# Kernel optimization log

Hardware: AMD Instinct MI355X
Metric: run time of the kernel (lower is better)

The kernel has to match this reference:

```python
import jax, jax.numpy as jnp
import numpy as np

V, D, L, H, S, B = 32000, 512, 4, 8, 2048, 2
HD = D // H
FF = 4 * D
EPS = 1e-5


def _ln(x, w, b):
    m = jnp.mean(x, axis=-1, keepdims=True)
    v = jnp.var(x, axis=-1, keepdims=True)
    return (x - m) / jnp.sqrt(v + EPS) * w + b


def setup_inputs() -> dict:
    key = jax.random.key(0)
    ks = jax.random.split(key, 32)
    rn = lambda k, shape, s=0.02: jax.random.normal(k, shape, jnp.float32) * s
    return {
        'x': jax.random.randint(ks[0], (B, S), 0, V),
        'tok_emb': rn(ks[1], (V, D)),
        'pos_emb': rn(ks[2], (S, D)),
        'qw': rn(ks[3], (L, D, D)), 'qb': rn(ks[4], (L, D)),
        'kw': rn(ks[5], (L, D, D)), 'kb': rn(ks[6], (L, D)),
        'vw': rn(ks[7], (L, D, D)), 'vb': rn(ks[8], (L, D)),
        'ow': rn(ks[9], (L, D, D)), 'ob': rn(ks[10], (L, D)),
        'qphase': rn(ks[11], (L, H), 0.1),
        'sp_phase': rn(ks[12], (L, D), 0.1),
        'n1w': jnp.ones((L, D), jnp.float32), 'n1b': jnp.zeros((L, D), jnp.float32),
        'n2w': jnp.ones((L, D), jnp.float32), 'n2b': jnp.zeros((L, D), jnp.float32),
        'f1w': rn(ks[13], (L, D, FF)), 'f1b': rn(ks[14], (L, FF)),
        'f2w': rn(ks[15], (L, FF, D)), 'f2b': rn(ks[16], (L, D)),
        'iw': rn(ks[17], (L, D, D)), 'ib': rn(ks[18], (L, D)),
        'gw': rn(ks[19], (L, D, D)), 'gb': rn(ks[20], (L, D)),
        'nw': jnp.ones((D,), jnp.float32), 'nb': jnp.zeros((D,), jnp.float32),
        'outw': rn(ks[21], (D, V)), 'outb': rn(ks[22], (V,)),
    }


def _forward(x, tok_emb, pos_emb, qw, qb, kw, kb, vw, vb, ow, ob, qphase, sp_phase,
             n1w, n1b, n2w, n2b, f1w, f1b, f2w, f2b, iw, ib, gw, gb, nw, nb, outw, outb):
    Bx, Sx = x.shape
    h = tok_emb[x] + pos_emb[:Sx][None, :, :]          # [B,S,D]
    mask = jnp.tril(jnp.ones((Sx, Sx), dtype=bool))    # causal
    scale = 1.0 / np.sqrt(HD).astype(np.float32)
    for l in range(L):
        # quantum attention with phase-modulated scores
        hn = _ln(h, n1w[l], n1b[l])
        q = (hn @ qw[l] + qb[l]).reshape(Bx, Sx, H, HD)
        k = (hn @ kw[l] + kb[l]).reshape(Bx, Sx, H, HD)
        v = (hn @ vw[l] + vb[l]).reshape(Bx, Sx, H, HD)
        scores = jnp.einsum('bqhd,bkhd->bhqk', q, k) * scale
        qi = jnp.cos(qphase[l][None, :, None, None] * scores)
        scores = scores * (1.0 + 0.1 * qi)
        scores = jnp.where(mask[None, None], scores, -jnp.inf)
        attn = jax.nn.softmax(scores, axis=-1)
        o = jnp.einsum('bhqk,bkhd->bqhd', attn, v).reshape(Bx, Sx, D)
        h = h + o @ ow[l] + ob[l]
        # superposition: x * cos(phase * x)
        h = h * jnp.cos(sp_phase[l] * h)
        # feed-forward (exact GELU, as torch default)
        hn2 = _ln(h, n2w[l], n2b[l])
        h = h + jax.nn.gelu(hn2 @ f1w[l] + f1b[l], approximate=False) @ f2w[l] + f2b[l]
        # interference gate
        g = jax.nn.sigmoid(h @ gw[l] + gb[l])
        h = (h @ iw[l] + ib[l]) * g + h * (1.0 - g)
    h = _ln(h, nw, nb)
    return h @ outw + outb                              # [B,S,V] logits


def reference(x, tok_emb, pos_emb, qw, qb, kw, kb, vw, vb, ow, ob, qphase, sp_phase,
              n1w, n1b, n2w, n2b, f1w, f1b, f2w, f2b, iw, ib, gw, gb, nw, nb, outw, outb):
    return _forward(x, tok_emb, pos_emb, qw, qb, kw, kb, vw, vb, ow, ob, qphase, sp_phase,
                    n1w, n1b, n2w, n2b, f1w, f1b, f2w, f2b, iw, ib, gw, gb, nw, nb, outw, outb)
```

## Files before the change

### kernel.cpp

```cpp
#include <hip/hip_runtime.h>
#include <math.h>

#define DIM 512
#define NH 8
#define HD 64
#define SEQ 2048
#define BATCH 2
#define NLAYER 4
#define FFD 2048
#define VOCAB 32000
#define ROWS (BATCH*SEQ)
#define QKV_LD 1536

typedef unsigned short u16;
typedef __attribute__((ext_vector_type(8))) short bfrag;
typedef __attribute__((ext_vector_type(4))) short sfrag4;
typedef __attribute__((ext_vector_type(4))) float facc;

__device__ __forceinline__ u16 f2bf(float f){
  unsigned u = __builtin_bit_cast(unsigned, f);
  u += 0x7fff + ((u>>16)&1);
  return (u16)(u>>16);
}

typedef __attribute__((address_space(3))) unsigned int lds_u32;
typedef const __attribute__((address_space(1))) unsigned int glob_u32;
__device__ __forceinline__ void gload16(const void* g, void* l){
  __builtin_amdgcn_global_load_lds((glob_u32*)g, (lds_u32*)l, 16, 0, 0);
}

template<int N> __device__ __forceinline__ void wait_vmcnt(){
  if constexpr (N==0)       asm volatile("s_waitcnt vmcnt(0)" ::: "memory");
  else if constexpr (N==3)  asm volatile("s_waitcnt vmcnt(3)" ::: "memory");
  else if constexpr (N==4)  asm volatile("s_waitcnt vmcnt(4)" ::: "memory");
  else if constexpr (N==6)  asm volatile("s_waitcnt vmcnt(6)" ::: "memory");
  else if constexpr (N==8)  asm volatile("s_waitcnt vmcnt(8)" ::: "memory");
  else if constexpr (N==16) asm volatile("s_waitcnt vmcnt(16)" ::: "memory");
  else static_assert(N==0, "unsupported vmcnt");
}

__device__ __forceinline__ void do_transpose(
    const float* __restrict__ I, u16* __restrict__ O,
    int K, int N, int nx, int ky, int imode){
  __shared__ float t[32][33];
  const int n0 = nx*32, k0 = ky*32;
  #pragma unroll
  for (int i=0;i<4;i++){
    int k = k0 + threadIdx.y + 8*i;
    t[threadIdx.y+8*i][threadIdx.x] = I[(size_t)k*N + n0 + threadIdx.x];
  }
  __syncthreads();
  #pragma unroll
  for (int i=0;i<4;i++){
    int n = n0 + threadIdx.y + 8*i;
    int np = (imode==0) ? n : ((n>>4)*32 + (n&15) + (imode==2 ? 16 : 0));
    O[(size_t)np*K + k0 + threadIdx.x] = f2bf(t[threadIdx.x][threadIdx.y+8*i]);
  }
}

__global__ void pre_all(
    const float* qw, const float* kw, const float* vw, const float* ow,
    const float* iw, const float* gw, const float* f1w, const float* f2w,
    const float* outw,
    const float* qb, const float* kb, const float* vb,
    const float* ib, const float* gb,
    u16* qkvT, u16* owT, u16* igT, u16* f1T, u16* f2T, u16* outT,
    float* qkvb, float* igb){
  const int bid = blockIdx.x;
  if (bid < 6144){
    int job = bid >> 10, local = bid & 1023;
    int l = local >> 8, rr = local & 255;
    int nx = rr & 15, ky = rr >> 4;
    const float* src; u16* dst; int im = 0;
    switch(job){
      case 0: src=qw+(size_t)l*262144; dst=qkvT+(size_t)l*786432;        break;
      case 1: src=kw+(size_t)l*262144; dst=qkvT+(size_t)l*786432+262144; break;
      case 2: src=vw+(size_t)l*262144; dst=qkvT+(size_t)l*786432+524288; break;
      case 3: src=ow+(size_t)l*262144; dst=owT +(size_t)l*262144;        break;
      case 4: src=iw+(size_t)l*262144; dst=igT +(size_t)l*524288; im=1;  break;
      default:src=gw+(size_t)l*262144; dst=igT +(size_t)l*524288; im=2;  break;
    }
    do_transpose(src, dst, 512, 512, nx, ky, im);
  } else if (bid < 10240){
    int local = bid - 6144;
    int l = local >> 10, rr = local & 1023;
    int nx = rr & 63, ky = rr >> 6;
    do_transpose(f1w+(size_t)l*1048576, f1T+(size_t)l*1048576, 512, 2048, nx, ky, 0);
  } else if (bid < 14336){
    int local = bid - 10240;
    int l = local >> 10, rr = local & 1023;
    int nx = rr & 15, ky = rr >> 4;
    do_transpose(f2w+(size_t)l*1048576, f2T+(size_t)l*1048576, 2048, 512, nx, ky, 0);
  } else if (bid < 30336){
    int local = bid - 14336;
    int nx = local % 1000, ky = local / 1000;
    do_transpose(outw, outT, 512, 32000, nx, ky, 0);
  } else if (bid < 30360){
    int tid = threadIdx.y*32 + threadIdx.x;
    int idx = (bid-30336)*256 + tid;
    int l = idx/1536, r2 = idx%1536;
    qkvb[idx] = (r2<512) ? qb[l*512+r2] : (r2<1024 ? kb[l*512+r2-512] : vb[l*512+r2-1024]);
  } else {
    int tid = threadIdx.y*32 + threadIdx.x;
    int idx = (bid-30360)*256 + tid;
    int l = idx>>10, cp = idx&1023;
    int bb = cp>>4, c = (bb>>1)*16 + (cp&15);
    igb[idx] = (bb&1) ? gb[l*512+c] : ib[l*512+c];
  }
}

__global__ void embed_k(const int* __restrict__ x, const float* __restrict__ tok,
                        const float* __restrict__ pos, float* __restrict__ h){
  int idx = blockIdx.x*256 + threadIdx.x;
  int row = idx >> 7;
  int d4  = idx & 127;
  int s   = row & (SEQ-1);
  int tkn = x[row];
  float4 tv = *(const float4*)(tok + (size_t)tkn*DIM + d4*4);
  float4 pv = *(const float4*)(pos + (size_t)s*DIM + d4*4);
  float4 r; r.x=tv.x+pv.x; r.y=tv.y+pv.y; r.z=tv.z+pv.z; r.w=tv.w+pv.w;
  *(float4*)(h + (size_t)row*DIM + d4*4) = r;
}

__global__ __launch_bounds__(256) void ln_k(const float* __restrict__ h,
    const float* __restrict__ w, const float* __restrict__ bsc,
    u16* __restrict__ out){
  const int wid = threadIdx.x>>6, lane = threadIdx.x&63;
  const int row = blockIdx.x*4 + wid;
  const float* r = h + (size_t)row*DIM + lane*8;
  float4 v0 = *(const float4*)r;
  float4 v1 = *(const float4*)(r+4);
  float s  = v0.x+v0.y+v0.z+v0.w + v1.x+v1.y+v1.z+v1.w;
  float ss = v0.x*v0.x+v0.y*v0.y+v0.z*v0.z+v0.w*v0.w
           + v1.x*v1.x+v1.y*v1.y+v1.z*v1.z+v1.w*v1.w;
  #pragma unroll
  for (int m=1;m<64;m<<=1){ s += __shfl_xor(s,m); ss += __shfl_xor(ss,m); }
  const float mean = s*(1.f/DIM);
  const float var  = ss*(1.f/DIM) - mean*mean;
  const float rsd  = rsqrtf(var + 1e-5f);
  float4 w0 = *(const float4*)(w + lane*8);
  float4 w1 = *(const float4*)(w + lane*8 + 4);
  float4 b0 = *(const float4*)(bsc + lane*8);
  float4 b1 = *(const float4*)(bsc + lane*8 + 4);
  bfrag pk;
  pk[0]=(short)f2bf((v0.x-mean)*rsd*w0.x+b0.x);
  pk[1]=(short)f2bf((v0.y-mean)*rsd*w0.y+b0.y);
  pk[2]=(short)f2bf((v0.z-mean)*rsd*w0.z+b0.z);
  pk[3]=(short)f2bf((v0.w-mean)*rsd*w0.w+b0.w);
  pk[4]=(short)f2bf((v1.x-mean)*rsd*w1.x+b1.x);
  pk[5]=(short)f2bf((v1.y-mean)*rsd*w1.y+b1.y);
  pk[6]=(short)f2bf((v1.z-mean)*rsd*w1.z+b1.z);
  pk[7]=(short)f2bf((v1.w-mean)*rsd*w1.w+b1.w);
  *(bfrag*)&out[(size_t)row*DIM + lane*8] = pk;
}

template<int BM,int BN,int BK,int WRN,int WCN,int DEPTH,int MODE,int SWZ>
__global__ __launch_bounds__(WRN*WCN*64, 2) void gemm_p(
    const u16* __restrict__ A, const u16* __restrict__ BT,
    const float* __restrict__ bias, const float* __restrict__ aux,
    float* __restrict__ Cf, u16* __restrict__ Cb, u16* __restrict__ vt,
    int M, int N, int K){
  constexpr int NTH = WRN*WCN*64;
  constexpr int FI  = BM/(16*WRN);
  constexpr int FJ  = BN/(16*WCN);
  constexpr int CPR = BK/8;
  constexpr int LA  = BM*CPR/NTH;
  constexpr int LB  = BN*CPR/NTH;
  constexpr int LPT = LA+LB;
  constexpr int NKK = BK/32;
  extern __shared__ __align__(16) u16 smem[];
  u16* lds_a = smem;
  u16* lds_b = smem + DEPTH*BM*BK;

  const int tid = threadIdx.x;
  const int wid = tid>>6, lane = tid&63;
  const int wr = wid / WCN, wc = wid % WCN;
  const int lr = lane&15, lg = lane>>4;
  int tm, tn;
  if constexpr (SWZ){
    const unsigned nwg = gridDim.x*gridDim.y;
    const unsigned lin = blockIdx.y*gridDim.x + blockIdx.x;
    const unsigned q = nwg >> 3;
    const unsigned sw = (lin & 7)*q + (lin >> 3);
    tm = sw % gridDim.x; tn = sw / gridDim.x;
  } else {
    tm = blockIdx.x; tn = blockIdx.y;
  }

  auto swzf = [](int row)->int{ return (BK==64) ? (row&7) : ((row>>1)&3); };

  auto stage = [&](int t, int buf){
    const int k0 = t*BK;
    #pragma unroll
    for (int i=0;i<LA;i++){
      int u = i*NTH + tid;
      int row = u/CPR, c = (u%CPR) ^ swzf(row);
      gload16(&A[(size_t)(tm*BM+row)*K + k0 + c*8], &lds_a[buf*BM*BK + u*8]);
    }
    #pragma unroll
    for (int i=0;i<LB;i++){
      int u = i*NTH + tid;
      int row = u/CPR, c = (u%CPR) ^ swzf(row);
      gload16(&BT[(size_t)(tn*BN+row)*K + k0 + c*8], &lds_b[buf*BN*BK + u*8]);
    }
  };

  facc acc[FI][FJ] = {};
  const int NT = K/BK;
  stage(0,0);
  if (NT>1) stage(1,1);
  if constexpr (DEPTH==3) { if (NT>2) stage(2,2); }
  for (int t=0;t<NT;t++){
    const int buf = t % DEPTH;
    const u16* la = &lds_a[buf*BM*BK];
    const u16* lb = &lds_b[buf*BN*BK];
    const int rem = NT-1-t;
    if constexpr (DEPTH==3){
      if (rem >= 2) wait_vmcnt<2*LPT>();
      else if (rem == 1) wait_vmcnt<LPT>();
      else wait_vmcnt<0>();
    } else {
      if (rem >= 1) wait_vmcnt<LPT>(); else wait_vmcnt<0>();
    }
    __builtin_amdgcn_s_barrier();
    __builtin_amdgcn_sched_barrier(0);
    bfrag af[FI], bf[FJ];
    #pragma unroll
    for (int i=0;i<FI;i++){
      int row = wr*(FI*16) + i*16 + lr;
      af[i] = *(const bfrag*)&la[row*BK + ((lg ^ swzf(row))*8)];
    }
    #pragma unroll
    for (int j=0;j<FJ;j++){
      int row = wc*(FJ*16) + j*16 + lr;
      bf[j] = *(const bfrag*)&lb[row*BK + ((lg ^ swzf(row))*8)];
    }
    if constexpr (NKK==1){
      asm volatile("s_waitcnt lgkmcnt(0)" ::: "memory");
      __builtin_amdgcn_sched_barrier(0);
      __builtin_amdgcn_s_barrier();
      __builtin_amdgcn_sched_barrier(0);
      if (t+DEPTH<NT) stage(t+DEPTH, buf);
      __builtin_amdgcn_s_setprio(1);
      #pragma unroll
      for (int i=0;i<FI;i++)
        #pragma unroll
        for (int j=0;j<FJ;j++)
          acc[i][j] = __builtin_amdgcn_mfma_f32_16x16x32_bf16(af[i], bf[j], acc[i][j],0,0,0);
      __builtin_amdgcn_s_setprio(0);
    } else {
      __builtin_amdgcn_s_setprio(1);
      #pragma unroll
      for (int i=0;i<FI;i++)
        #pragma unroll
        for (int j=0;j<FJ;j++)
          acc[i][j] = __builtin_amdgcn_mfma_f32_16x16x32_bf16(af[i], bf[j], acc[i][j],0,0,0);
      __builtin_amdgcn_s_setprio(0);
      bfrag af1[FI], bf1[FJ];
      #pragma unroll
      for (int i=0;i<FI;i++){
        int row = wr*(FI*16) + i*16 + lr;
        af1[i] = *(const bfrag*)&la[row*BK + (((4+lg) ^ swzf(row))*8)];
      }
      #pragma unroll
      for (int j=0;j<FJ;j++){
        int row = wc*(FJ*16) + j*16 + lr;
        bf1[j] = *(const bfrag*)&lb[row*BK + (((4+lg) ^ swzf(row))*8)];
      }
      asm volatile("s_waitcnt lgkmcnt(0)" ::: "memory");
      __builtin_amdgcn_sched_barrier(0);
      __builtin_amdgcn_s_barrier();
      __builtin_amdgcn_sched_barrier(0);
      if (t+DEPTH<NT) stage(t+DEPTH, buf);
      __builtin_amdgcn_s_setprio(1);
      #pragma unroll
      for (int i=0;i<FI;i++)
        #pragma unroll
        for (int j=0;j<FJ;j++)
          acc[i][j] = __builtin_amdgcn_mfma_f32_16x16x32_bf16(af1[i], bf1[j], acc[i][j],0,0,0);
      __builtin_amdgcn_s_setprio(0);
    }
  }

  if constexpr (MODE==5){
    #pragma unroll
    for (int i=0;i<FI;i++){
      #pragma unroll
      for (int j=0;j<FJ;j+=2){
        const int colp = tn*BN + wc*(FJ*16) + j*16;
        const int c = (colp>>5)*16 + lr;
        const float bi = bias[colp + lr];
        const float bg = bias[colp + 16 + lr];
        #pragma unroll
        for (int r=0;r<4;r++){
          const int row = tm*BM + wr*(FI*16) + i*16 + lg*4 + r;
          float vi = acc[i][j][r]   + bi;
          float vg = acc[i][j+1][r] + bg;
          float g  = 1.f/(1.f+__expf(-vg));
          const size_t o = (size_t)row*DIM + c;
          float hv = Cf[o];
          Cf[o] = vi*g + hv*(1.f-g);
        }
      }
    }
  } else if constexpr (MODE==7){
    #pragma unroll
    for (int i=0;i<FI;i++){
      #pragma unroll
      for (int j=0;j<FJ;j++){
        const int colblk = tn*BN + wc*(FJ*16) + j*16;
        const float bv = bias[colblk + lr];
        if (colblk < 1024){
          #pragma unroll
          for (int r=0;r<4;r++){
            const int row = tm*BM + wr*(FI*16) + i*16 + lg*4 + r;
            Cb[(size_t)row*N + colblk + lr] = f2bf(acc[i][j][r] + bv);
          }
        } else {
          const int c = colblk + lr - 1024;
          const int hh = c>>6, d = c&63;
          const int row0 = tm*BM + wr*(FI*16) + i*16 + lg*4;
          const int b = row0>>11, s0 = row0&2047;
          sfrag4 pk;
          #pragma unroll
          for (int r=0;r<4;r++) pk[r] = (short)f2bf(acc[i][j][r] + bv);
          *(sfrag4*)&vt[((size_t)((b*NH+hh)*HD + d))*SEQ + s0] = pk;
        }
      }
    }
  } else {
    #pragma unroll
    for (int i=0;i<FI;i++){
      #pragma unroll
      for (int j=0;j<FJ;j++){
        const int col = tn*BN + wc*(FJ*16) + j*16 + lr;
        const float bv = bias ? bias[col] : 0.f;
        #pragma unroll
        for (int r=0;r<4;r++){
          const int row = tm*BM + wr*(FI*16) + i*16 + lg*4 + r;
          float v = acc[i][j][r] + bv;
          const size_t o = (size_t)row*N + col;
          if      (MODE==0) Cf[o] = v;
          else if (MODE==8) __builtin_nontemporal_store(v, &Cf[o]);
          else if (MODE==3){ float g = 0.5f*v*(1.f+erff(v*0.70710678118f)); Cb[o] = f2bf(g); }
          else if (MODE==4){ float t = Cf[o] + v; t = t*__cosf(aux[col]*t); Cf[o] = t; }
          else if (MODE==6){ float t = Cf[o] + v; Cf[o] = t; Cb[o] = f2bf(t); }
        }
      }
    }
  }
}

__global__ __launch_bounds__(256) void attn_k(
    const u16* __restrict__ QKV, const u16* __restrict__ VT,
    const float* __restrict__ qphase, u16* __restrict__ O){
  __shared__ __align__(16) u16 lds_p[4][16*32];
  const int qblk = blockIdx.x, hh = blockIdx.y, b = blockIdx.z;
  const int tid = threadIdx.x;
  const int wid = tid>>6, lane = tid&63;
  const int lr = lane&15, lg = lane>>4;
  const int qbase = qblk*64 + wid*16;
  const float ph = qphase[hh];
  const float scale = 0.125f;
  u16* pbuf = lds_p[wid];

  bfrag aq[2];
  #pragma unroll
  for (int st=0; st<2; st++)
    aq[st] = *(const bfrag*)&QKV[(size_t)(b*SEQ + qbase + lr)*QKV_LD + hh*HD + st*32 + lg*8];

  facc oacc[4];
  #pragma unroll
  for (int n=0;n<4;n++) oacc[n] = (facc){0.f,0.f,0.f,0.f};
  float lrow[4] = {0.f,0.f,0.f,0.f};

  const int nkv = (qbase + 15)/32 + 1;
  for (int kt=0; kt<nkv; kt++){
    const int kv0 = kt*32;
    facc sc[2];
    #pragma unroll
    for (int j=0;j<2;j++){
      bfrag bk0 = *(const bfrag*)&QKV[(size_t)(b*SEQ + kv0 + j*16 + lr)*QKV_LD + 512 + hh*HD + lg*8];
      bfrag bk1 = *(const bfrag*)&QKV[(size_t)(b*SEQ + kv0 + j*16 + lr)*QKV_LD + 512 + hh*HD + 32 + lg*8];
      facc z = (facc){0.f,0.f,0.f,0.f};
      z     = __builtin_amdgcn_mfma_f32_16x16x32_bf16(aq[0], bk0, z, 0,0,0);
      sc[j] = __builtin_amdgcn_mfma_f32_16x16x32_bf16(aq[1], bk1, z, 0,0,0);
    }
    bfrag vbf[4];
    #pragma unroll
    for (int n=0;n<4;n++)
      vbf[n] = *(const bfrag*)&VT[((size_t)((b*NH + hh)*HD + n*16 + lr))*SEQ + kv0 + lg*8];

    float pv[2][4];
    #pragma unroll
    for (int j=0;j<2;j++)
      #pragma unroll
      for (int r=0;r<4;r++){
        int srow = qbase + lg*4 + r;
        int scol = kv0 + j*16 + lr;
        float xv = sc[j][r]*scale;
        xv = xv*(1.f + 0.1f*__cosf(ph*xv));
        if (scol > srow) xv = -1e30f;
        pv[j][r] = __expf(xv);
      }
    #pragma unroll
    for (int r=0;r<4;r++){
      float rs = pv[0][r] + pv[1][r];
      rs += __shfl_xor(rs,1);
      rs += __shfl_xor(rs,2);
      rs += __shfl_xor(rs,4);
      rs += __shfl_xor(rs,8);
      lrow[r] += rs;
    }
    #pragma unroll
    for (int j=0;j<2;j++)
      #pragma unroll
      for (int r=0;r<4;r++)
        pbuf[(lg*4+r)*32 + j*16 + lr] = f2bf(pv[j][r]);
    bfrag pa = *(const bfrag*)&pbuf[lr*32 + lg*8];
    #pragma unroll
    for (int n=0;n<4;n++)
      oacc[n] = __builtin_amdgcn_mfma_f32_16x16x32_bf16(pa, vbf[n], oacc[n], 0,0,0);
  }
  float rcp[4];
  #pragma unroll
  for (int r=0;r<4;r++) rcp[r] = 1.f/lrow[r];
  #pragma unroll
  for (int n=0;n<4;n++)
    #pragma unroll
    for (int r=0;r<4;r++){
      float val = oacc[n][r] * rcp[r];
      O[(size_t)(b*SEQ + qbase + lg*4 + r)*DIM + hh*HD + n*16 + lr] = f2bf(val);
    }
}

extern "C" void kernel_launch(void* const* d_in, const int* in_sizes, int n_in,
                              void* d_out, int out_size, void* d_ws, size_t ws_size,
                              hipStream_t stream){
  const int*   x        = (const int*)d_in[0];
  const float* tok_emb  = (const float*)d_in[1];
  const float* pos_emb  = (const float*)d_in[2];
  const float* qw = (const float*)d_in[3];  const float* qb = (const float*)d_in[4];
  const float* kw = (const float*)d_in[5];  const float* kb = (const float*)d_in[6];
  const float* vw = (const float*)d_in[7];  const float* vb = (const float*)d_in[8];
  const float* ow = (const float*)d_in[9];  const float* ob = (const float*)d_in[10];
  const float* qphase   = (const float*)d_in[11];
  const float* sp_phase = (const float*)d_in[12];
  const float* n1w = (const float*)d_in[13]; const float* n1b = (const float*)d_in[14];
  const float* n2w = (const float*)d_in[15]; const float* n2b = (const float*)d_in[16];
  const float* f1w = (const float*)d_in[17]; const float* f1b = (const float*)d_in[18];
  const float* f2w = (const float*)d_in[19]; const float* f2b = (const float*)d_in[20];
  const float* iw  = (const float*)d_in[21]; const float* ib  = (const float*)d_in[22];
  const float* gw  = (const float*)d_in[23]; const float* gb  = (const float*)d_in[24];
  const float* nw  = (const float*)d_in[25]; const float* nb  = (const float*)d_in[26];
  const float* outw= (const float*)d_in[27]; const float* outb= (const float*)d_in[28];
  float* out = (float*)d_out;

  char* base = (char*)d_ws;
  size_t off = 0;
  auto alloc = [&](size_t bytes)->void*{
    void* p = base + off; off += bytes; off = (off + 255) & ~(size_t)255; return p;
  };
  float* h    = (float*)alloc((size_t)ROWS*DIM*4);
  u16* hn     = (u16*)alloc((size_t)ROWS*DIM*2);
  u16* qkvB   = (u16*)alloc((size_t)ROWS*QKV_LD*2);
  u16* vTb    = (u16*)alloc((size_t)ROWS*DIM*2);
  u16* oB     = (u16*)alloc((size_t)ROWS*DIM*2);
  u16* hB     = (u16*)alloc((size_t)ROWS*DIM*2);
  u16* ffB    = (u16*)alloc((size_t)ROWS*FFD*2);
  u16* qkvT = (u16*)alloc((size_t)NLAYER*1536*DIM*2);
  u16* owT  = (u16*)alloc((size_t)NLAYER*DIM*DIM*2);
  u16* igT  = (u16*)alloc((size_t)NLAYER*1024*DIM*2);
  u16* f1T  = (u16*)alloc((size_t)NLAYER*DIM*FFD*2);
  u16* f2T  = (u16*)alloc((size_t)NLAYER*DIM*FFD*2);
  u16* outT = (u16*)alloc((size_t)VOCAB*DIM*2);
  float* qkvb = (float*)alloc((size_t)NLAYER*1536*4);
  float* igb  = (float*)alloc((size_t)NLAYER*1024*4);

  dim3 tb(32,8);
  pre_all<<<30376, tb, 0, stream>>>(qw,kw,vw,ow,iw,gw,f1w,f2w,outw,
                                    qb,kb,vb,ib,gb,
                                    qkvT,owT,igT,f1T,f2T,outT, qkvb,igb);
  embed_k<<<ROWS*DIM/4/256, 256, 0, stream>>>(x, tok_emb, pos_emb, h);

  constexpr size_t SM_MID3 = 3*(128+128)*32*2;
  constexpr size_t SM_ROW3 = 3*(64+128)*32*2;
  constexpr size_t SM_VOC3 = 3*(128+128)*32*2;

  for (int l=0;l<NLAYER;l++){
    ln_k<<<ROWS/4, 256, 0, stream>>>(h, n1w + l*DIM, n1b + l*DIM, hn);
    gemm_p<128,128,32,2,2,3,7,1><<<dim3(ROWS/128, 1536/128), 256, SM_MID3, stream>>>(
        hn, qkvT + (size_t)l*1536*DIM, qkvb + l*1536, nullptr,
        nullptr, qkvB, vTb, ROWS, 1536, DIM);
    attn_k<<<dim3(SEQ/64, NH, BATCH), 256, 0, stream>>>(qkvB, vTb, qphase + l*NH, oB);
    gemm_p<64,128,32,1,4,3,4,1><<<dim3(ROWS/64, DIM/128), 256, SM_ROW3, stream>>>(
        oB, owT + (size_t)l*DIM*DIM, ob + l*DIM, sp_phase + l*DIM,
        h, nullptr, nullptr, ROWS, DIM, DIM);
    ln_k<<<ROWS/4, 256, 0, stream>>>(h, n2w + l*DIM, n2b + l*DIM, hn);
    gemm_p<128,128,32,2,2,3,3,1><<<dim3(ROWS/128, FFD/128), 256, SM_MID3, stream>>>(
        hn, f1T + (size_t)l*DIM*FFD, f1b + l*FFD, nullptr,
        nullptr, ffB, nullptr, ROWS, FFD, DIM);
    gemm_p<64,128,32,1,4,3,6,1><<<dim3(ROWS/64, DIM/128), 256, SM_ROW3, stream>>>(
        ffB, f2T + (size_t)l*DIM*FFD, f2b + l*DIM, nullptr,
        h, hB, nullptr, ROWS, DIM, FFD);
    gemm_p<64,128,32,1,4,3,5,1><<<dim3(ROWS/64, 1024/128), 256, SM_ROW3, stream>>>(
        hB, igT + (size_t)l*1024*DIM, igb + l*1024, nullptr,
        h, nullptr, nullptr, ROWS, 1024, DIM);
  }
  ln_k<<<ROWS/4, 256, 0, stream>>>(h, nw, nb, hn);
  gemm_p<128,128,32,2,2,3,8,0><<<dim3(ROWS/128, VOCAB/128), 256, SM_VOC3, stream>>>(
      hn, outT, outb, nullptr, out, nullptr, nullptr, ROWS, VOCAB, DIM);
}
```

Measured before the change: 1.053 ms.

## Fuse LayerNorm apply into GEMM A-tile loading using precomputed row stats

Replaces the full LayerNorm kernel, which wrote a bf16 normalized copy, with a small stats kernel that stores per-row mean and rsqrt-variance. The QKV, FF1 and vocab GEMMs then read fp32 h directly and normalize and convert it while staging A tiles into LDS, with the stats for the block's rows held in shared memory. This removes the bf16 intermediate write and read. In exchange, A loads become synchronous register loads instead of async global-to-LDS copies, which weakens load/compute overlap, and every column tile re-reads fp32 A at twice the bytes of bf16. It also drops the unused BK=64 path.

```diff
diff --git a/kernel.cpp b/kernel.cpp
--- a/kernel.cpp
+++ b/kernel.cpp
@@ -31,11 +31,11 @@
 
 template<int N> __device__ __forceinline__ void wait_vmcnt(){
   if constexpr (N==0)       asm volatile("s_waitcnt vmcnt(0)" ::: "memory");
+  else if constexpr (N==2)  asm volatile("s_waitcnt vmcnt(2)" ::: "memory");
   else if constexpr (N==3)  asm volatile("s_waitcnt vmcnt(3)" ::: "memory");
   else if constexpr (N==4)  asm volatile("s_waitcnt vmcnt(4)" ::: "memory");
   else if constexpr (N==6)  asm volatile("s_waitcnt vmcnt(6)" ::: "memory");
   else if constexpr (N==8)  asm volatile("s_waitcnt vmcnt(8)" ::: "memory");
-  else if constexpr (N==16) asm volatile("s_waitcnt vmcnt(16)" ::: "memory");
   else static_assert(N==0, "unsupported vmcnt");
 }
 
@@ -122,9 +122,8 @@
   *(float4*)(h + (size_t)row*DIM + d4*4) = r;
 }
 
-__global__ __launch_bounds__(256) void ln_k(const float* __restrict__ h,
-    const float* __restrict__ w, const float* __restrict__ bsc,
-    u16* __restrict__ out){
+__global__ __launch_bounds__(256) void ln_stat_k(const float* __restrict__ h,
+    float* __restrict__ stg){
   const int wid = threadIdx.x>>6, lane = threadIdx.x&63;
   const int row = blockIdx.x*4 + wid;
   const float* r = h + (size_t)row*DIM + lane*8;
@@ -135,30 +134,21 @@
            + v1.x*v1.x+v1.y*v1.y+v1.z*v1.z+v1.w*v1.w;
   #pragma unroll
   for (int m=1;m<64;m<<=1){ s += __shfl_xor(s,m); ss += __shfl_xor(ss,m); }
-  const float mean = s*(1.f/DIM);
-  const float var  = ss*(1.f/DIM) - mean*mean;
-  const float rsd  = rsqrtf(var + 1e-5f);
-  float4 w0 = *(const float4*)(w + lane*8);
-  float4 w1 = *(const float4*)(w + lane*8 + 4);
-  float4 b0 = *(const float4*)(bsc + lane*8);
-  float4 b1 = *(const float4*)(bsc + lane*8 + 4);
-  bfrag pk;
-  pk[0]=(short)f2bf((v0.x-mean)*rsd*w0.x+b0.x);
-  pk[1]=(short)f2bf((v0.y-mean)*rsd*w0.y+b0.y);
-  pk[2]=(short)f2bf((v0.z-mean)*rsd*w0.z+b0.z);
-  pk[3]=(short)f2bf((v0.w-mean)*rsd*w0.w+b0.w);
-  pk[4]=(short)f2bf((v1.x-mean)*rsd*w1.x+b1.x);
-  pk[5]=(short)f2bf((v1.y-mean)*rsd*w1.y+b1.y);
-  pk[6]=(short)f2bf((v1.z-mean)*rsd*w1.z+b1.z);
-  pk[7]=(short)f2bf((v1.w-mean)*rsd*w1.w+b1.w);
-  *(bfrag*)&out[(size_t)row*DIM + lane*8] = pk;
-}
-
-template<int BM,int BN,int BK,int WRN,int WCN,int DEPTH,int MODE,int SWZ>
+  if (lane==0){
+    const float mean = s*(1.f/DIM);
+    const float var  = ss*(1.f/DIM) - mean*mean;
+    stg[row*2]   = mean;
+    stg[row*2+1] = rsqrtf(var + 1e-5f);
+  }
+}
+
+template<int BM,int BN,int BK,int WRN,int WCN,int DEPTH,int MODE,int SWZ,int LNF>
 __global__ __launch_bounds__(WRN*WCN*64, 2) void gemm_p(
     const u16* __restrict__ A, const u16* __restrict__ BT,
     const float* __restrict__ bias, const float* __restrict__ aux,
     float* __restrict__ Cf, u16* __restrict__ Cb, u16* __restrict__ vt,
+    const float* __restrict__ Af, const float* __restrict__ lnw,
+    const float* __restrict__ lnb, const float* __restrict__ stg,
     int M, int N, int K){
   constexpr int NTH = WRN*WCN*64;
   constexpr int FI  = BM/(16*WRN);
@@ -166,11 +156,12 @@
   constexpr int CPR = BK/8;
   constexpr int LA  = BM*CPR/NTH;
   constexpr int LB  = BN*CPR/NTH;
-  constexpr int LPT = LA+LB;
+  constexpr int LPTW = LNF ? LB : (LA+LB);
   constexpr int NKK = BK/32;
   extern __shared__ __align__(16) u16 smem[];
   u16* lds_a = smem;
   u16* lds_b = smem + DEPTH*BM*BK;
+  float* stf = (float*)(smem + DEPTH*(BM+BN)*BK);
 
   const int tid = threadIdx.x;
   const int wid = tid>>6, lane = tid&63;
@@ -189,13 +180,45 @@
 
   auto swzf = [](int row)->int{ return (BK==64) ? (row&7) : ((row>>1)&3); };
 
+  if constexpr (LNF){
+    if (tid < BM){
+      float2 st = *(const float2*)&stg[(size_t)(tm*BM+tid)*2];
+      stf[tid*2]   = st.x;
+      stf[tid*2+1] = st.y;
+    }
+    __syncthreads();
+  }
+
   auto stage = [&](int t, int buf){
     const int k0 = t*BK;
-    #pragma unroll
-    for (int i=0;i<LA;i++){
-      int u = i*NTH + tid;
-      int row = u/CPR, c = (u%CPR) ^ swzf(row);
-      gload16(&A[(size_t)(tm*BM+row)*K + k0 + c*8], &lds_a[buf*BM*BK + u*8]);
+    if constexpr (LNF){
+      #pragma unroll
+      for (int i=0;i<LA;i++){
+        int u = i*NTH + tid;
+        int row = u/CPR, c = (u%CPR) ^ swzf(row);
+        const float* src = Af + (size_t)(tm*BM+row)*K + k0 + c*8;
+        float4 a0 = *(const float4*)src, a1 = *(const float4*)(src+4);
+        float4 w0 = *(const float4*)(lnw + k0 + c*8), w1 = *(const float4*)(lnw + k0 + c*8 + 4);
+        float4 b0 = *(const float4*)(lnb + k0 + c*8), b1 = *(const float4*)(lnb + k0 + c*8 + 4);
+        const float mu = stf[row*2], rs = stf[row*2+1];
+        bfrag pk;
+        pk[0]=(short)f2bf((a0.x-mu)*rs*w0.x+b0.x);
+        pk[1]=(short)f2bf((a0.y-mu)*rs*w0.y+b0.y);
+        pk[2]=(short)f2bf((a0.z-mu)*rs*w0.z+b0.z);
+        pk[3]=(short)f2bf((a0.w-mu)*rs*w0.w+b0.w);
+        pk[4]=(short)f2bf((a1.x-mu)*rs*w1.x+b1.x);
+        pk[5]=(short)f2bf((a1.y-mu)*rs*w1.y+b1.y);
+        pk[6]=(short)f2bf((a1.z-mu)*rs*w1.z+b1.z);
+        pk[7]=(short)f2bf((a1.w-mu)*rs*w1.w+b1.w);
+        *(bfrag*)&lds_a[buf*BM*BK + u*8] = pk;
+      }
+    } else {
+      #pragma unroll
+      for (int i=0;i<LA;i++){
+        int u = i*NTH + tid;
+        int row = u/CPR, c = (u%CPR) ^ swzf(row);
+        gload16(&A[(size_t)(tm*BM+row)*K + k0 + c*8], &lds_a[buf*BM*BK + u*8]);
+      }
     }
     #pragma unroll
     for (int i=0;i<LB;i++){
@@ -210,17 +233,21 @@
   stage(0,0);
   if (NT>1) stage(1,1);
   if constexpr (DEPTH==3) { if (NT>2) stage(2,2); }
+  if constexpr (LNF){
+    asm volatile("s_waitcnt lgkmcnt(0)" ::: "memory");
+    __builtin_amdgcn_sched_barrier(0);
+  }
   for (int t=0;t<NT;t++){
     const int buf = t % DEPTH;
     const u16* la = &lds_a[buf*BM*BK];
     const u16* lb = &lds_b[buf*BN*BK];
     const int rem = NT-1-t;
     if constexpr (DEPTH==3){
-      if (rem >= 2) wait_vmcnt<2*LPT>();
-      else if (rem == 1) wait_vmcnt<LPT>();
+      if (rem >= 2) wait_vmcnt<2*LPTW>();
+      else if (rem == 1) wait_vmcnt<LPTW>();
       else wait_vmcnt<0>();
     } else {
-      if (rem >= 1) wait_vmcnt<LPT>(); else wait_vmcnt<0>();
+      if (rem >= 1) wait_vmcnt<LPTW>(); else wait_vmcnt<0>();
     }
     __builtin_amdgcn_s_barrier();
     __builtin_amdgcn_sched_barrier(0);
@@ -235,51 +262,18 @@
       int row = wc*(FJ*16) + j*16 + lr;
       bf[j] = *(const bfrag*)&lb[row*BK + ((lg ^ swzf(row))*8)];
     }
-    if constexpr (NKK==1){
-      asm volatile("s_waitcnt lgkmcnt(0)" ::: "memory");
-      __builtin_amdgcn_sched_barrier(0);
-      __builtin_amdgcn_s_barrier();
-      __builtin_amdgcn_sched_barrier(0);
-      if (t+DEPTH<NT) stage(t+DEPTH, buf);
-      __builtin_amdgcn_s_setprio(1);
-      #pragma unroll
-      for (int i=0;i<FI;i++)
-        #pragma unroll
-        for (int j=0;j<FJ;j++)
-          acc[i][j] = __builtin_amdgcn_mfma_f32_16x16x32_bf16(af[i], bf[j], acc[i][j],0,0,0);
-      __builtin_amdgcn_s_setprio(0);
-    } else {
-      __builtin_amdgcn_s_setprio(1);
-      #pragma unroll
-      for (int i=0;i<FI;i++)
-        #pragma unroll
-        for (int j=0;j<FJ;j++)
-          acc[i][j] = __builtin_amdgcn_mfma_f32_16x16x32_bf16(af[i], bf[j], acc[i][j],0,0,0);
-      __builtin_amdgcn_s_setprio(0);
-      bfrag af1[FI], bf1[FJ];
-      #pragma unroll
-      for (int i=0;i<FI;i++){
-        int row = wr*(FI*16) + i*16 + lr;
-        af1[i] = *(const bfrag*)&la[row*BK + (((4+lg) ^ swzf(row))*8)];
-      }
-      #pragma unroll
-      for (int j=0;j<FJ;j++){
-        int row = wc*(FJ*16) + j*16 + lr;
-        bf1[j] = *(const bfrag*)&lb[row*BK + (((4+lg) ^ swzf(row))*8)];
-      }
-      asm volatile("s_waitcnt lgkmcnt(0)" ::: "memory");
-      __builtin_amdgcn_sched_barrier(0);
-      __builtin_amdgcn_s_barrier();
-      __builtin_amdgcn_sched_barrier(0);
-      if (t+DEPTH<NT) stage(t+DEPTH, buf);
-      __builtin_amdgcn_s_setprio(1);
-      #pragma unroll
-      for (int i=0;i<FI;i++)
-        #pragma unroll
-        for (int j=0;j<FJ;j++)
-          acc[i][j] = __builtin_amdgcn_mfma_f32_16x16x32_bf16(af1[i], bf1[j], acc[i][j],0,0,0);
-      __builtin_amdgcn_s_setprio(0);
-    }
+    asm volatile("s_waitcnt lgkmcnt(0)" ::: "memory");
+    __builtin_amdgcn_sched_barrier(0);
+    __builtin_amdgcn_s_barrier();
+    __builtin_amdgcn_sched_barrier(0);
+    if (t+DEPTH<NT) stage(t+DEPTH, buf);
+    __builtin_amdgcn_s_setprio(1);
+    #pragma unroll
+    for (int i=0;i<FI;i++)
+      #pragma unroll
+      for (int j=0;j<FJ;j++)
+        acc[i][j] = __builtin_amdgcn_mfma_f32_16x16x32_bf16(af[i], bf[j], acc[i][j],0,0,0);
+    __builtin_amdgcn_s_setprio(0);
   }
 
   if constexpr (MODE==5){
@@ -462,7 +456,7 @@
     void* p = base + off; off += bytes; off = (off + 255) & ~(size_t)255; return p;
   };
   float* h    = (float*)alloc((size_t)ROWS*DIM*4);
-  u16* hn     = (u16*)alloc((size_t)ROWS*DIM*2);
+  float* stg  = (float*)alloc((size_t)ROWS*2*4);
   u16* qkvB   = (u16*)alloc((size_t)ROWS*QKV_LD*2);
   u16* vTb    = (u16*)alloc((size_t)ROWS*DIM*2);
   u16* oB     = (u16*)alloc((size_t)ROWS*DIM*2);
@@ -483,31 +477,33 @@
                                     qkvT,owT,igT,f1T,f2T,outT, qkvb,igb);
   embed_k<<<ROWS*DIM/4/256, 256, 0, stream>>>(x, tok_emb, pos_emb, h);
 
-  constexpr size_t SM_MID3 = 3*(128+128)*32*2;
-  constexpr size_t SM_ROW3 = 3*(64+128)*32*2;
-  constexpr size_t SM_VOC3 = 3*(128+128)*32*2;
+  constexpr size_t SM_MID3  = 3*(128+128)*32*2;
+  constexpr size_t SM_MID3L = SM_MID3 + 128*2*4;
+  constexpr size_t SM_ROW3  = 3*(64+128)*32*2;
+  constexpr size_t SM_VOC3L = 3*(128+128)*32*2 + 128*2*4;
 
   for (int l=0;l<NLAYER;l++){
-    ln_k<<<ROWS/4, 256, 0, stream>>>(h, n1w + l*DIM, n1b + l*DIM, hn);
-    gemm_p<128,128,32,2,2,3,7,1><<<dim3(ROWS/128, 1536/128), 256, SM_MID3, stream>>>(
-        hn, qkvT + (size_t)l*1536*DIM, qkvb + l*1536, nullptr,
-        nullptr, qkvB, vTb, ROWS, 1536, DIM);
+    ln_stat_k<<<ROWS/4, 256, 0, stream>>>(h, stg);
+    gemm_p<128,128,32,2,2,3,7,1,1><<<dim3(ROWS/128, 1536/128), 256, SM_MID3L, stream>>>(
+        nullptr, qkvT + (size_t)l*1536*DIM, qkvb + l*1536, nullptr,
+        nullptr, qkvB, vTb, h, n1w + l*DIM, n1b + l*DIM, stg, ROWS, 1536, DIM);
     attn_k<<<dim3(SEQ/64, NH, BATCH), 256, 0, stream>>>(qkvB, vTb, qphase + l*NH, oB);
-    gemm_p<64,128,32,1,4,3,4,1><<<dim3(ROWS/64, DIM/128), 256, SM_ROW3, stream>>>(
+    gemm_p<64,128,32,1,4,3,4,1,0><<<dim3(ROWS/64, DIM/128), 256, SM_ROW3, stream>>>(
         oB, owT + (size_t)l*DIM*DIM, ob + l*DIM, sp_phase + l*DIM,
-        h, nullptr, nullptr, ROWS, DIM, DIM);
-    ln_k<<<ROWS/4, 256, 0, stream>>>(h, n2w + l*DIM, n2b + l*DIM, hn);
-    gemm_p<128,128,32,2,2,3,3,1><<<dim3(ROWS/128, FFD/128), 256, SM_MID3, stream>>>(
-        hn, f1T + (size_t)l*DIM*FFD, f1b + l*FFD, nullptr,
-        nullptr, ffB, nullptr, ROWS, FFD, DIM);
-    gemm_p<64,128,32,1,4,3,6,1><<<dim3(ROWS/64, DIM/128), 256, SM_ROW3, stream>>>(
+        h, nullptr, nullptr, nullptr, nullptr, nullptr, nullptr, ROWS, DIM, DIM);
+    ln_stat_k<<<ROWS/4, 256, 0, stream>>>(h, stg);
+    gemm_p<128,128,32,2,2,3,3,1,1><<<dim3(ROWS/128, FFD/128), 256, SM_MID3L, stream>>>(
+        nullptr, f1T + (size_t)l*DIM*FFD, f1b + l*FFD, nullptr,
+        nullptr, ffB, nullptr, h, n2w + l*DIM, n2b + l*DIM, stg, ROWS, FFD, DIM);
+    gemm_p<64,128,32,1,4,3,6,1,0><<<dim3(ROWS/64, DIM/128), 256, SM_ROW3, stream>>>(
         ffB, f2T + (size_t)l*DIM*FFD, f2b + l*DIM, nullptr,
-        h, hB, nullptr, ROWS, DIM, FFD);
-    gemm_p<64,128,32,1,4,3,5,1><<<dim3(ROWS/64, 1024/128), 256, SM_ROW3, stream>>>(
+        h, hB, nullptr, nullptr, nullptr, nullptr, nullptr, ROWS, DIM, FFD);
+    gemm_p<64,128,32,1,4,3,5,1,0><<<dim3(ROWS/64, 1024/128), 256, SM_ROW3, stream>>>(
         hB, igT + (size_t)l*1024*DIM, igb + l*1024, nullptr,
-        h, nullptr, nullptr, ROWS, 1024, DIM);
-  }
-  ln_k<<<ROWS/4, 256, 0, stream>>>(h, nw, nb, hn);
-  gemm_p<128,128,32,2,2,3,8,0><<<dim3(ROWS/128, VOCAB/128), 256, SM_VOC3, stream>>>(
-      hn, outT, outb, nullptr, out, nullptr, nullptr, ROWS, VOCAB, DIM);
-}
+        h, nullptr, nullptr, nullptr, nullptr, nullptr, nullptr, ROWS, 1024, DIM);
+  }
+  ln_stat_k<<<ROWS/4, 256, 0, stream>>>(h, stg);
+  gemm_p<128,128,32,2,2,3,8,0,1><<<dim3(ROWS/128, VOCAB/128), 256, SM_VOC3L, stream>>>(
+      nullptr, outT, outb, nullptr, out, nullptr, nullptr,
+      h, nw, nb, stg, ROWS, VOCAB, DIM);
+}
```

Result: slower. 1.205 ms (+14.5%).
